# Performance work log

Hardware: AMD Instinct MI355X
Metric: run time of the kernel (lower is better)

The kernel has to match this reference:

```python
import jax, jax.numpy as jnp
import numpy as np

B, N, D, H = 128, 512, 128, 8
DH = D // H
CLIP = 10.0          # tanh_clipping
NEG = -1.0e9         # finite -inf for masking (keeps grads clean)


def setup_inputs() -> dict:
    key = jax.random.key(0)
    ks = jax.random.split(key, 6)
    s = 0.08  # ~1/sqrt(D) init scale so pre-tanh logits are in a sane range
    return {
        "embeddings": jax.random.normal(ks[0], (B, N, D), jnp.float32),
        "W_node_proj": jax.random.normal(ks[1], (D, 3 * D), jnp.float32) * s,
        "W_fixed_ctx": jax.random.normal(ks[2], (D, D), jnp.float32) * s,
        "W_step_ctx": jax.random.normal(ks[3], (2 * D, D), jnp.float32) * s,
        "W_out": jax.random.normal(ks[4], (D, D), jnp.float32) * s,
        "W_placeholder": jax.random.uniform(ks[5], (2 * D,), jnp.float32, -1.0, 1.0),
    }


def reference(embeddings, W_node_proj, W_fixed_ctx, W_step_ctx, W_out, W_placeholder):
    # _precompute: fixed context + glimpse K/V + logit key (cached for all steps)
    graph_embed = embeddings.mean(axis=1)                    # [B,D]
    fixed_ctx = graph_embed @ W_fixed_ctx                    # [B,D]
    proj = embeddings @ W_node_proj                          # [B,N,3D]
    gK, gV, logit_K = jnp.split(proj, 3, axis=-1)
    gK = gK.reshape(B, N, H, DH)                             # glimpse key heads
    gV = gV.reshape(B, N, H, DH)                             # glimpse val heads
    inv_sqrt_dh = 1.0 / jnp.sqrt(jnp.float32(DH))
    inv_sqrt_d = 1.0 / jnp.sqrt(jnp.float32(D))
    batch_idx = jnp.arange(B)

    def step(carry, _):
        visited, first, prev, i = carry
        # step context: placeholder at i==0, else concat(first, current) embeddings
        cur_ctx = jnp.concatenate(
            [embeddings[batch_idx, first], embeddings[batch_idx, prev]], axis=-1)  # [B,2D]
        step_ctx = jnp.where(i == 0, W_placeholder[None, :], cur_ctx)
        q = fixed_ctx + step_ctx @ W_step_ctx                # [B,D]
        qh = q.reshape(B, H, DH)
        # masked multi-head glimpse attention
        compat = jnp.einsum('bhd,bnhd->bhn', qh, gK) * inv_sqrt_dh
        compat = jnp.where(visited[:, None, :], NEG, compat)
        attn = jax.nn.softmax(compat, axis=-1)
        heads = jnp.einsum('bhn,bnhd->bhd', attn, gV)
        glimpse = heads.reshape(B, D) @ W_out                # project_out
        # logit attention with tanh clipping
        logits = jnp.einsum('bd,bnd->bn', glimpse, logit_K) * inv_sqrt_d
        logits = CLIP * jnp.tanh(logits)
        logits = jnp.where(visited, NEG, logits)
        log_p = jax.nn.log_softmax(logits, axis=-1)
        sel = jnp.argmax(log_p, axis=-1).astype(jnp.int32)   # greedy decode
        visited = visited.at[batch_idx, sel].set(True)
        first = jnp.where(i == 0, sel, first)
        return (visited, first, sel, i + 1), (log_p, sel)

    init = (jnp.zeros((B, N), bool), jnp.zeros((B,), jnp.int32),
            jnp.zeros((B,), jnp.int32), jnp.int32(0))
    _, (log_ps, pis) = jax.lax.scan(step, init, None, length=N)
    log_p = jnp.transpose(log_ps, (1, 0, 2))                 # [B,N_steps,N]
    pi = jnp.transpose(pis, (1, 0))                          # [B,N_steps]
    # _calc_log_likelihood
    ll = jnp.take_along_axis(log_p, pi[:, :, None], axis=2).squeeze(-1).sum(axis=1)
    return log_p, pi, ll
```

## Files before the change

### kernel.cpp

```cpp
#include <hip/hip_runtime.h>
#include <hip/hip_bf16.h>
#include <math.h>

#define BATCH 128
#define NN 512
#define DD 128
#define D3 384
#define NEGV (-1.0e9f)
#define NEGINF (-1.0e30f)

__global__ __launch_bounds__(256) void k_fixed(const float* __restrict__ emb,
                                               const float* __restrict__ Wf,
                                               const float* __restrict__ Wstep,
                                               const float* __restrict__ Wph,
                                               float* __restrict__ fixedc,
                                               float* __restrict__ q0) {
  const int b = blockIdx.x;
  __shared__ float s_part[2][DD];
  __shared__ float s_ge[DD];
  const int tid = threadIdx.x;
  const int d = tid & 127, c = tid >> 7;
  const float* e = emb + (size_t)b * NN * DD;
  float acc = 0.f;
  for (int n = c * 256; n < c * 256 + 256; ++n) acc += e[(size_t)n * DD + d];
  s_part[c][d] = acc;
  __syncthreads();
  if (tid < DD) s_ge[tid] = (s_part[0][tid] + s_part[1][tid]) * (1.0f / 512.0f);
  __syncthreads();
  if (tid < DD) {
    float a = 0.f;
    for (int k = 0; k < DD; ++k) a += s_ge[k] * Wf[k * DD + tid];
    fixedc[b * DD + tid] = a;
    float pq = 0.f;
    for (int k = 0; k < 2 * DD; ++k) pq += Wph[k] * Wstep[k * DD + tid];
    q0[b * DD + tid] = a + pq;
  }
}

__global__ __launch_bounds__(384) void k_proj(const float* __restrict__ emb,
                                              const float* __restrict__ Wp,
                                              float* __restrict__ proj) {
  const size_t row0 = (size_t)blockIdx.x * 32;
  __shared__ float s_A[32][DD];
  const int tid = threadIdx.x;
  for (int t = tid; t < 32 * DD; t += 384)
    s_A[t >> 7][t & 127] = emb[row0 * DD + t];
  __syncthreads();
  float acc[32];
#pragma unroll
  for (int r = 0; r < 32; ++r) acc[r] = 0.f;
  const int c = tid;
  for (int k = 0; k < DD; ++k) {
    float w = Wp[k * D3 + c];
#pragma unroll
    for (int r = 0; r < 32; ++r) acc[r] += s_A[r][k] * w;
  }
  for (int r = 0; r < 32; ++r) proj[(row0 + r) * D3 + c] = acc[r];
}

__global__ __launch_bounds__(128) void k_lp(float* __restrict__ proj,
                                            const float* __restrict__ Wout) {
  const size_t row0 = (size_t)blockIdx.x * 32;
  __shared__ float s_L[32][DD];
  const int tid = threadIdx.x;
  for (int rr = 0; rr < 32; ++rr)
    s_L[rr][tid] = proj[(row0 + rr) * D3 + 2 * DD + tid];
  __syncthreads();
  float acc[32];
#pragma unroll
  for (int r = 0; r < 32; ++r) acc[r] = 0.f;
  for (int d = 0; d < DD; ++d) {
    const float w = Wout[tid * DD + d];
#pragma unroll
    for (int r = 0; r < 32; ++r) acc[r] += w * s_L[r][d];
  }
  for (int r = 0; r < 32; ++r)
    proj[(row0 + r) * D3 + 2 * DD + tid] = acc[r];
}

__global__ __launch_bounds__(256) void k_ectx(const float* __restrict__ emb,
                                              const float* __restrict__ Wstep,
                                              float* __restrict__ E12) {
  const size_t row0 = (size_t)blockIdx.x * 32;
  __shared__ float s_A[32][DD];
  const int tid = threadIdx.x;
  for (int t = tid; t < 32 * DD; t += 256)
    s_A[t >> 7][t & 127] = emb[row0 * DD + t];
  __syncthreads();
  float acc[32];
#pragma unroll
  for (int r = 0; r < 32; ++r) acc[r] = 0.f;
  const int c = tid;
  const float* wp = (c < DD) ? (Wstep + c) : (Wstep + DD * DD + (c - DD));
  for (int k = 0; k < DD; ++k) {
    float w = wp[(size_t)k * DD];
#pragma unroll
    for (int r = 0; r < 32; ++r) acc[r] += s_A[r][k] * w;
  }
  for (int r = 0; r < 32; ++r) E12[(row0 + r) * 256 + c] = acc[r];
}

__global__ __launch_bounds__(1024, 1) void k_decode(
    const float* __restrict__ emb, const float* __restrict__ proj,
    const float* __restrict__ fixedc, const float* __restrict__ q0,
    const float* __restrict__ E12, const float* __restrict__ Wstep,
    const float* __restrict__ Wph, const int useE, float* __restrict__ out) {
  const int b = blockIdx.x;
  const int tid = threadIdx.x;
  const int lane = tid & 63;
  const int wave = tid >> 6;
  const int h = tid & 7, r = tid >> 3;

  __shared__ int s_idx[NN];
  __shared__ int s_pos[NN];
  __shared__ unsigned char s_visited[NN];
  __shared__ float s_hacc[16][8][17];
  __shared__ float s_heads[DD];
  __shared__ float s_logits[NN];
  __shared__ float s_rm[16];
  __shared__ int s_ri[16];
  __shared__ float s_es[16];
  __shared__ float s_q[DD];
  __shared__ float s_ctx[2 * DD];
  __shared__ int s_first, s_prev, s_M;
  __shared__ float s_ll;

  const float inv_sqrt_d = 0.08838834764831845f;
  const size_t eb = (size_t)b * NN * DD;
  const size_t e2 = (size_t)b * NN * 256;
  const float* projb = proj + (size_t)b * NN * D3;
  float* outp = out + (size_t)b * NN * NN;
  const size_t PI_OFF = (size_t)BATCH * NN * NN;
  const size_t LL_OFF = PI_OFF + (size_t)BATCH * NN;

  float f16[16];
#pragma unroll
  for (int d = 0; d < 4; ++d) {
    const float4 v = *(const float4*)(fixedc + b * DD + h * 16 + d * 4);
    f16[d * 4 + 0] = v.x; f16[d * 4 + 1] = v.y;
    f16[d * 4 + 2] = v.z; f16[d * 4 + 3] = v.w;
  }

  if (tid < NN) {
    s_idx[tid] = tid;
    s_pos[tid] = tid;
    s_visited[tid] = 0;
  }
  if (tid == 0) { s_first = 0; s_prev = 0; s_ll = 0.f; s_M = NN; }
  __syncthreads();

  for (int i = 0; i < NN; ++i) {
    const int M = s_M;
    const int first = s_first, prev = s_prev;

    float qf[16];
    if (useE) {
      if (i == 0) {
#pragma unroll
        for (int d = 0; d < 4; ++d) {
          const float4 v = *(const float4*)(q0 + b * DD + h * 16 + d * 4);
          qf[d * 4 + 0] = v.x; qf[d * 4 + 1] = v.y;
          qf[d * 4 + 2] = v.z; qf[d * 4 + 3] = v.w;
        }
      } else {
        const float* e1p = E12 + e2 + (size_t)first * 256 + h * 16;
        const float* e2p = E12 + e2 + (size_t)prev * 256 + DD + h * 16;
#pragma unroll
        for (int d = 0; d < 4; ++d) {
          const float4 a = *(const float4*)(e1p + d * 4);
          const float4 c = *(const float4*)(e2p + d * 4);
          qf[d * 4 + 0] = f16[d * 4 + 0] + a.x + c.x;
          qf[d * 4 + 1] = f16[d * 4 + 1] + a.y + c.y;
          qf[d * 4 + 2] = f16[d * 4 + 2] + a.z + c.z;
          qf[d * 4 + 3] = f16[d * 4 + 3] + a.w + c.w;
        }
      }
    } else {
      if (tid < 2 * DD) {
        float v;
        if (i == 0)
          v = Wph[tid];
        else
          v = (tid < DD) ? emb[eb + (size_t)first * DD + tid]
                         : emb[eb + (size_t)prev * DD + (tid - DD)];
        s_ctx[tid] = v;
      }
      __syncthreads();
      if (tid < DD) {
        float a = fixedc[b * DD + tid];
        for (int k = 0; k < 2 * DD; ++k) a += s_ctx[k] * Wstep[k * DD + tid];
        s_q[tid] = a;
      }
      __syncthreads();
#pragma unroll
      for (int d = 0; d < 16; ++d) qf[d] = s_q[h * 16 + d];
    }

    bool act[4];
    int nj[4];
#pragma unroll
    for (int k = 0; k < 4; ++k) {
      const int j = r + k * 128;
      act[k] = (j < M);
      nj[k] = s_idx[j];
    }
    float s_l = 0.f;
    float acc[16];
#pragma unroll
    for (int d = 0; d < 16; ++d) acc[d] = 0.f;
#pragma unroll
    for (int k = 0; k < 4; ++k) {
      if (act[k]) {
        const float* rp = projb + (size_t)nj[k] * D3 + h * 16;
        const float4* kp = (const float4*)rp;
        float4 k0 = kp[0], k1 = kp[1], k2 = kp[2], k3 = kp[3];
        float a = qf[0] * k0.x + qf[1] * k0.y + qf[2] * k0.z + qf[3] * k0.w +
                  qf[4] * k1.x + qf[5] * k1.y + qf[6] * k1.z + qf[7] * k1.w +
                  qf[8] * k2.x + qf[9] * k2.y + qf[10] * k2.z + qf[11] * k2.w +
                  qf[12] * k3.x + qf[13] * k3.y + qf[14] * k3.z +
                  qf[15] * k3.w;
        const float p = expf(a * 0.25f);
        s_l += p;
        const float4* vp = (const float4*)(rp + DD);
        float4 v0 = vp[0], v1 = vp[1], v2 = vp[2], v3 = vp[3];
        acc[0] += p * v0.x;  acc[1] += p * v0.y;
        acc[2] += p * v0.z;  acc[3] += p * v0.w;
        acc[4] += p * v1.x;  acc[5] += p * v1.y;
        acc[6] += p * v1.z;  acc[7] += p * v1.w;
        acc[8] += p * v2.x;  acc[9] += p * v2.y;
        acc[10] += p * v2.z; acc[11] += p * v2.w;
        acc[12] += p * v3.x; acc[13] += p * v3.y;
        acc[14] += p * v3.z; acc[15] += p * v3.w;
      }
    }
    {
      const bool k1 = (lane & 8) == 0;
#pragma unroll
      for (int d = 0; d < 8; ++d) {
        const float send = k1 ? acc[d + 8] : acc[d];
        const float got = __shfl_xor(send, 8);
        acc[d] = (k1 ? acc[d] : acc[d + 8]) + got;
      }
      const bool k2 = (lane & 16) == 0;
#pragma unroll
      for (int d = 0; d < 4; ++d) {
        const float send = k2 ? acc[d + 4] : acc[d];
        const float got = __shfl_xor(send, 16);
        acc[d] = (k2 ? acc[d] : acc[d + 4]) + got;
      }
      const bool k3 = (lane & 32) == 0;
#pragma unroll
      for (int d = 0; d < 2; ++d) {
        const float send = k3 ? acc[d + 2] : acc[d];
        const float got = __shfl_xor(send, 32);
        acc[d] = (k3 ? acc[d] : acc[d + 2]) + got;
      }
    }
    s_l += __shfl_xor(s_l, 8);
    s_l += __shfl_xor(s_l, 16);
    s_l += __shfl_xor(s_l, 32);
    {
      const int dim0 = ((lane & 8) ? 8 : 0) | ((lane & 16) ? 4 : 0) |
                       ((lane & 32) ? 2 : 0);
      s_hacc[wave][h][dim0] = acc[0];
      s_hacc[wave][h][dim0 + 1] = acc[1];
      if (lane < 8) s_hacc[wave][lane][16] = s_l;
    }
    if (tid >= 512) {
      const int t2 = tid - 512;
      if (s_visited[t2]) s_logits[t2] = NEGV;
    }
    __syncthreads();

    if (tid < DD) {
      const int hh = tid >> 4, dh = tid & 15;
      float num = 0.f, den = 0.f;
#pragma unroll
      for (int w = 0; w < 16; ++w) {
        num += s_hacc[w][hh][dh];
        den += s_hacc[w][hh][16];
      }
      s_heads[tid] = num / den;
    }
    __syncthreads();

    float gf[16];
#pragma unroll
    for (int d = 0; d < 16; ++d) gf[d] = s_heads[h * 16 + d];
    float av = NEGINF;
    int ai = 0x7FFFFFFF;
    float asum = 0.f;
#pragma unroll
    for (int k = 0; k < 4; ++k) {
      if (act[k]) {
        const float4* lp =
            (const float4*)(projb + (size_t)nj[k] * D3 + 2 * DD + h * 16);
        float4 l0 = lp[0], l1 = lp[1], l2 = lp[2], l3 = lp[3];
        float a = gf[0] * l0.x + gf[1] * l0.y + gf[2] * l0.z + gf[3] * l0.w +
                  gf[4] * l1.x + gf[5] * l1.y + gf[6] * l1.z + gf[7] * l1.w +
                  gf[8] * l2.x + gf[9] * l2.y + gf[10] * l2.z + gf[11] * l2.w +
                  gf[12] * l3.x + gf[13] * l3.y + gf[14] * l3.z +
                  gf[15] * l3.w;
        a += __shfl_xor(a, 1);
        a += __shfl_xor(a, 2);
        a += __shfl_xor(a, 4);
        if (h == 0) {
          const float lg = 10.0f * tanhf(a * inv_sqrt_d);
          s_logits[nj[k]] = lg;
          asum += expf(lg);
          if (lg > av || (lg == av && nj[k] < ai)) { av = lg; ai = nj[k]; }
        }
      }
    }
#pragma unroll
    for (int off = 1; off <= 32; off <<= 1) {
      const float ov = __shfl_xor(av, off);
      const int oi = __shfl_xor(ai, off);
      asum += __shfl_xor(asum, off);
      if (ov > av || (ov == av && oi < ai)) { av = ov; ai = oi; }
    }
    if (lane == 0) { s_rm[wave] = av; s_ri[wave] = ai; s_es[wave] = asum; }
    __syncthreads();

    float bv = s_rm[0];
    int bi = s_ri[0];
    float bs = s_es[0];
#pragma unroll
    for (int w2 = 1; w2 < 16; ++w2) {
      const float ov = s_rm[w2];
      const int oi = s_ri[w2];
      bs += s_es[w2];
      if (ov > bv || (ov == bv && oi < bi)) { bv = ov; bi = oi; }
    }
    const float lz = logf(bs);
    const int sel = bi;
    if (tid < NN) outp[(size_t)i * NN + tid] = s_logits[tid] - lz;
    if (tid == 0) {
      s_ll += s_logits[sel] - lz;
      s_visited[sel] = 1;
      if (i == 0) s_first = sel;
      s_prev = sel;
      out[PI_OFF + (size_t)b * NN + i] = (float)sel;
      const int p = s_pos[sel];
      const int last = s_idx[M - 1];
      s_idx[p] = last;
      s_pos[last] = p;
      s_idx[M - 1] = sel;
      s_pos[sel] = M - 1;
      s_M = M - 1;
    }
    __syncthreads();
  }
  if (tid == 0) out[LL_OFF + b] = s_ll;
}

extern "C" void kernel_launch(void* const* d_in, const int* in_sizes, int n_in,
                              void* d_out, int out_size, void* d_ws,
                              size_t ws_size, hipStream_t stream) {
  const float* emb = (const float*)d_in[0];
  const float* Wnp = (const float*)d_in[1];
  const float* Wf = (const float*)d_in[2];
  const float* Wstep = (const float*)d_in[3];
  const float* Wout = (const float*)d_in[4];
  const float* Wph = (const float*)d_in[5];
  float* out = (float*)d_out;

  const size_t projN = (size_t)BATCH * NN * D3;
  const size_t eN = (size_t)BATCH * NN * 256;
  const size_t need_full = (projN + eN + 2 * (size_t)BATCH * DD) * 4;

  float* proj = (float*)d_ws;
  float* E12 = proj + projN;
  const int useE = (ws_size >= need_full) ? 1 : 0;
  float* fixedc = useE ? (E12 + eN) : (proj + projN);
  float* q0 = fixedc + (size_t)BATCH * DD;

  k_fixed<<<BATCH, 256, 0, stream>>>(emb, Wf, Wstep, Wph, fixedc, q0);
  k_proj<<<(BATCH * NN) / 32, 384, 0, stream>>>(emb, Wnp, proj);
  k_lp<<<(BATCH * NN) / 32, 128, 0, stream>>>(proj, Wout);
  if (useE) k_ectx<<<(BATCH * NN) / 32, 256, 0, stream>>>(emb, Wstep, E12);
  k_decode<<<BATCH, 1024, 0, stream>>>(emb, proj, fixedc, q0,
                                       useE ? E12 : nullptr, Wstep, Wph, useE,
                                       out);
}
```

Measured before the change: 6.463 ms.

## Cache logit keys for first two compacted slots in LDS; fold fixed context into E12

Stores the logit-key vectors for the first 256 compacted active-node positions in shared memory (128 KB) and reads them from there in the decode loop. After each step, the one slot changed by the swap-remove is refreshed from global memory. The fixed-context vector is added into the precomputed E12 table so the decode kernel no longer keeps it in registers. This trades a large LDS footprint and an extra refresh load per step for fewer global reads in the per-step logit computation.

```diff
diff --git a/kernel.cpp b/kernel.cpp
--- a/kernel.cpp
+++ b/kernel.cpp
@@ -80,6 +80,7 @@
 
 __global__ __launch_bounds__(256) void k_ectx(const float* __restrict__ emb,
                                               const float* __restrict__ Wstep,
+                                              const float* __restrict__ fixedc,
                                               float* __restrict__ E12) {
   const size_t row0 = (size_t)blockIdx.x * 32;
   __shared__ float s_A[32][DD];
@@ -91,14 +92,43 @@
 #pragma unroll
   for (int r = 0; r < 32; ++r) acc[r] = 0.f;
   const int c = tid;
+  const int b = (int)(row0 >> 9);
   const float* wp = (c < DD) ? (Wstep + c) : (Wstep + DD * DD + (c - DD));
   for (int k = 0; k < DD; ++k) {
     float w = wp[(size_t)k * DD];
 #pragma unroll
     for (int r = 0; r < 32; ++r) acc[r] += s_A[r][k] * w;
   }
-  for (int r = 0; r < 32; ++r) E12[(row0 + r) * 256 + c] = acc[r];
-}
+  const float fc = (c < DD) ? fixedc[b * DD + c] : 0.f;
+  for (int r = 0; r < 32; ++r) E12[(row0 + r) * 256 + c] = acc[r] + fc;
+}
+
+#define DOT16(q, F)                                                           \
+  (q[0] * F[0].x + q[1] * F[0].y + q[2] * F[0].z + q[3] * F[0].w +            \
+   q[4] * F[1].x + q[5] * F[1].y + q[6] * F[1].z + q[7] * F[1].w +            \
+   q[8] * F[2].x + q[9] * F[2].y + q[10] * F[2].z + q[11] * F[2].w +          \
+   q[12] * F[3].x + q[13] * F[3].y + q[14] * F[3].z + q[15] * F[3].w)
+
+#define L_LOAD(njx, Lr)                                                       \
+  {                                                                           \
+    const float4* lp_ =                                                       \
+        (const float4*)(projb + (size_t)(njx)*D3 + 2 * DD + h * 16);          \
+    Lr[0] = lp_[0]; Lr[1] = lp_[1]; Lr[2] = lp_[2]; Lr[3] = lp_[3];           \
+  }
+
+#define L_CONSUME(Lr, njx)                                                    \
+  {                                                                           \
+    float a_ = DOT16(gf, Lr);                                                 \
+    a_ += __shfl_xor(a_, 1);                                                  \
+    a_ += __shfl_xor(a_, 2);                                                  \
+    a_ += __shfl_xor(a_, 4);                                                  \
+    if (h == 0) {                                                             \
+      const float lg_ = 10.0f * tanhf(a_ * inv_sqrt_d);                       \
+      s_logits[njx] = lg_;                                                    \
+      asum += expf(lg_);                                                      \
+      if (lg_ > av || (lg_ == av && (njx) < ai)) { av = lg_; ai = (njx); }    \
+    }                                                                         \
+  }
 
 __global__ __launch_bounds__(1024, 1) void k_decode(
     const float* __restrict__ emb, const float* __restrict__ proj,
@@ -111,6 +141,7 @@
   const int wave = tid >> 6;
   const int h = tid & 7, r = tid >> 3;
 
+  __shared__ float4 s_Lpf[2][4][16][64];
   __shared__ int s_idx[NN];
   __shared__ int s_pos[NN];
   __shared__ unsigned char s_visited[NN];
@@ -122,7 +153,7 @@
   __shared__ float s_es[16];
   __shared__ float s_q[DD];
   __shared__ float s_ctx[2 * DD];
-  __shared__ int s_first, s_prev, s_M;
+  __shared__ int s_first, s_prev, s_M, s_swap;
   __shared__ float s_ll;
 
   const float inv_sqrt_d = 0.08838834764831845f;
@@ -133,20 +164,21 @@
   const size_t PI_OFF = (size_t)BATCH * NN * NN;
   const size_t LL_OFF = PI_OFF + (size_t)BATCH * NN;
 
-  float f16[16];
-#pragma unroll
-  for (int d = 0; d < 4; ++d) {
-    const float4 v = *(const float4*)(fixedc + b * DD + h * 16 + d * 4);
-    f16[d * 4 + 0] = v.x; f16[d * 4 + 1] = v.y;
-    f16[d * 4 + 2] = v.z; f16[d * 4 + 3] = v.w;
-  }
-
   if (tid < NN) {
     s_idx[tid] = tid;
     s_pos[tid] = tid;
     s_visited[tid] = 0;
   }
   if (tid == 0) { s_first = 0; s_prev = 0; s_ll = 0.f; s_M = NN; }
+#pragma unroll
+  for (int s = 0; s < 2; ++s) {
+    const float4* lp =
+        (const float4*)(projb + (size_t)(r + s * 128) * D3 + 2 * DD + h * 16);
+    s_Lpf[s][0][wave][lane] = lp[0];
+    s_Lpf[s][1][wave][lane] = lp[1];
+    s_Lpf[s][2][wave][lane] = lp[2];
+    s_Lpf[s][3][wave][lane] = lp[3];
+  }
   __syncthreads();
 
   for (int i = 0; i < NN; ++i) {
@@ -169,10 +201,10 @@
         for (int d = 0; d < 4; ++d) {
           const float4 a = *(const float4*)(e1p + d * 4);
           const float4 c = *(const float4*)(e2p + d * 4);
-          qf[d * 4 + 0] = f16[d * 4 + 0] + a.x + c.x;
-          qf[d * 4 + 1] = f16[d * 4 + 1] + a.y + c.y;
-          qf[d * 4 + 2] = f16[d * 4 + 2] + a.z + c.z;
-          qf[d * 4 + 3] = f16[d * 4 + 3] + a.w + c.w;
+          qf[d * 4 + 0] = a.x + c.x;
+          qf[d * 4 + 1] = a.y + c.y;
+          qf[d * 4 + 2] = a.z + c.z;
+          qf[d * 4 + 3] = a.w + c.w;
         }
       }
     } else {
@@ -290,27 +322,31 @@
     float av = NEGINF;
     int ai = 0x7FFFFFFF;
     float asum = 0.f;
-#pragma unroll
-    for (int k = 0; k < 4; ++k) {
-      if (act[k]) {
-        const float4* lp =
-            (const float4*)(projb + (size_t)nj[k] * D3 + 2 * DD + h * 16);
-        float4 l0 = lp[0], l1 = lp[1], l2 = lp[2], l3 = lp[3];
-        float a = gf[0] * l0.x + gf[1] * l0.y + gf[2] * l0.z + gf[3] * l0.w +
-                  gf[4] * l1.x + gf[5] * l1.y + gf[6] * l1.z + gf[7] * l1.w +
-                  gf[8] * l2.x + gf[9] * l2.y + gf[10] * l2.z + gf[11] * l2.w +
-                  gf[12] * l3.x + gf[13] * l3.y + gf[14] * l3.z +
-                  gf[15] * l3.w;
-        a += __shfl_xor(a, 1);
-        a += __shfl_xor(a, 2);
-        a += __shfl_xor(a, 4);
-        if (h == 0) {
-          const float lg = 10.0f * tanhf(a * inv_sqrt_d);
-          s_logits[nj[k]] = lg;
-          asum += expf(lg);
-          if (lg > av || (lg == av && nj[k] < ai)) { av = lg; ai = nj[k]; }
-        }
-      }
+    if (act[0]) {
+      float4 LA[4];
+      LA[0] = s_Lpf[0][0][wave][lane];
+      LA[1] = s_Lpf[0][1][wave][lane];
+      LA[2] = s_Lpf[0][2][wave][lane];
+      LA[3] = s_Lpf[0][3][wave][lane];
+      L_CONSUME(LA, nj[0]);
+    }
+    if (act[1]) {
+      float4 LA[4];
+      LA[0] = s_Lpf[1][0][wave][lane];
+      LA[1] = s_Lpf[1][1][wave][lane];
+      LA[2] = s_Lpf[1][2][wave][lane];
+      LA[3] = s_Lpf[1][3][wave][lane];
+      L_CONSUME(LA, nj[1]);
+    }
+    if (act[2]) {
+      float4 LA[4];
+      L_LOAD(nj[2], LA);
+      L_CONSUME(LA, nj[2]);
+    }
+    if (act[3]) {
+      float4 LA[4];
+      L_LOAD(nj[3], LA);
+      L_CONSUME(LA, nj[3]);
     }
 #pragma unroll
     for (int off = 1; off <= 32; off <<= 1) {
@@ -348,8 +384,23 @@
       s_idx[M - 1] = sel;
       s_pos[sel] = M - 1;
       s_M = M - 1;
+      s_swap = p;
     }
     __syncthreads();
+
+    {
+      const int sp = s_swap;
+      if (sp < 256 && r == (sp & 127)) {
+        const int sl = sp >> 7;
+        const int nr = s_idx[sp];
+        const float4* lp =
+            (const float4*)(projb + (size_t)nr * D3 + 2 * DD + h * 16);
+        s_Lpf[sl][0][wave][lane] = lp[0];
+        s_Lpf[sl][1][wave][lane] = lp[1];
+        s_Lpf[sl][2][wave][lane] = lp[2];
+        s_Lpf[sl][3][wave][lane] = lp[3];
+      }
+    }
   }
   if (tid == 0) out[LL_OFF + b] = s_ll;
 }
@@ -378,7 +429,7 @@
   k_fixed<<<BATCH, 256, 0, stream>>>(emb, Wf, Wstep, Wph, fixedc, q0);
   k_proj<<<(BATCH * NN) / 32, 384, 0, stream>>>(emb, Wnp, proj);
   k_lp<<<(BATCH * NN) / 32, 128, 0, stream>>>(proj, Wout);
-  if (useE) k_ectx<<<(BATCH * NN) / 32, 256, 0, stream>>>(emb, Wstep, E12);
+  if (useE) k_ectx<<<(BATCH * NN) / 32, 256, 0, stream>>>(emb, Wstep, fixedc, E12);
   k_decode<<<BATCH, 1024, 0, stream>>>(emb, proj, fixedc, q0,
                                        useE ? E12 : nullptr, Wstep, Wph, useE,
                                        out);
```

Measured after the change: 5.802 ms, median of 2. 10.2% less time.
